# Kernel tuning notes

Hardware: AMD Instinct MI355X
Metric: run time of the kernel (lower is better)

The kernel has to match this reference:

```python
import jax, jax.numpy as jnp
import numpy as np

EPS = 1e-5

def setup_inputs() -> dict:
    key = jax.random.key(0)
    k1, k2 = jax.random.split(key)
    N, D = 8192, 256
    q_features = jax.random.normal(k1, (N, D), dtype=jnp.float32)
    g_features = jax.random.normal(k2, (N, D), dtype=jnp.float32)
    return {"q_features": q_features, "g_features": g_features}

def reference(q_features, g_features):
    # logits[i, j] = q_i . g_j ; original computes row i as g_features @ q_i
    logits = jnp.einsum('id,jd->ij', q_features, g_features)  # [N, N]
    # exp(l_ii)/sum_j exp(l_ij) == softmax row diagonal (stable form, same math)
    probs_diag = jnp.diagonal(jax.nn.softmax(logits, axis=-1))  # [N]
    loss = jnp.mean(-jnp.log(probs_diag + EPS))
    return loss
```

## Files before the change

kernel.cpp:

```cpp
#include <hip/hip_runtime.h>
#include <stdint.h>


#define LOG2E 1.44269504f
#define KOFF  92.3324826f

typedef __attribute__((ext_vector_type(8))) short short8;
typedef __attribute__((ext_vector_type(4))) float f32x4;

__device__ __forceinline__ uint32_t pack2bf(float lo, float hi) {
    return __builtin_amdgcn_perm(__float_as_uint(hi), __float_as_uint(lo), 0x07060302u);
}

__global__ __launch_bounds__(256) void k_cvt(const float* __restrict__ q,
                                             const float* __restrict__ g,
                                             uint4* __restrict__ qb,
                                             uint4* __restrict__ gb) {
    int o = blockIdx.x * 256 + threadIdx.x;
    const float* src = q;
    uint4* dst = qb;
    float s = LOG2E;
    if (o >= 262144) { o -= 262144; src = g; dst = gb; s = 1.0f; }
    int p   = o >> 11;
    int b   = (o >> 6) & 31;
    int l   = o & 63;
    int row = p * 64 + (b & 3) * 16 + (l & 15);
    int k0  = (b >> 2) * 32 + (l >> 4) * 8;
    const float4* sp = (const float4*)(src + row * 256 + k0);
    float4 a = sp[0], c = sp[1];
    uint4 ov;
    ov.x = pack2bf(a.x * s, a.y * s); ov.y = pack2bf(a.z * s, a.w * s);
    ov.z = pack2bf(c.x * s, c.y * s); ov.w = pack2bf(c.z * s, c.w * s);
    dst[o] = ov;
}

__global__ __launch_bounds__(256, 2) void k_main(const uint4* __restrict__ qb,
                                                 const uint4* __restrict__ gb,
                                                 float* __restrict__ zpart,
                                                 float* __restrict__ diag) {
    const int tid  = threadIdx.x;
    const int wave = tid >> 6;
    const int lane = tid & 63;
    const int l15  = lane & 15;
    const int quad = lane >> 4;
    const int t    = blockIdx.x >> 4;
    const int cs   = blockIdx.x & 15;
    const int rowbase = t * 256 + wave * 64;

    short8 afrag[4][8];
    {
        const char* qp = (const char*)qb + (size_t)(t * 4 + wave) * 32768 + (lane << 4);
#pragma unroll
        for (int rg = 0; rg < 4; ++rg)
#pragma unroll
            for (int ks = 0; ks < 8; ++ks)
                afrag[rg][ks] = *(const short8*)(qp + ((ks * 4 + rg) << 10));
    }

    float zacc[4][4];
#pragma unroll
    for (int rg = 0; rg < 4; ++rg)
#pragma unroll
        for (int r = 0; r < 4; ++r) zacc[rg][r] = 0.f;

    const bool bd = (cs == (t >> 1));

    for (int jt = 0; jt < 8; ++jt) {
        const char* gp = (const char*)gb + (size_t)(cs * 8 + jt) * 32768 + (lane << 4);

        f32x4 acc[4][4];
#pragma unroll
        for (int rg = 0; rg < 4; ++rg)
#pragma unroll
            for (int cf = 0; cf < 4; ++cf) acc[rg][cf] = (f32x4){0.f, 0.f, 0.f, 0.f};

#pragma unroll
        for (int ks = 0; ks < 8; ++ks)
#pragma unroll
            for (int cf = 0; cf < 4; ++cf) {
                short8 b = *(const short8*)(gp + ((ks * 4 + cf) << 10));
#pragma unroll
                for (int rg = 0; rg < 4; ++rg)
                    acc[rg][cf] = __builtin_amdgcn_mfma_f32_16x16x32_bf16(
                        afrag[rg][ks], b, acc[rg][cf], 0, 0, 0);
            }

#pragma unroll
        for (int rg = 0; rg < 4; ++rg)
#pragma unroll
            for (int r = 0; r < 4; ++r) {
                float e0 = __builtin_amdgcn_exp2f(acc[rg][0][r] - KOFF);
                float e1 = __builtin_amdgcn_exp2f(acc[rg][1][r] - KOFF);
                float e2 = __builtin_amdgcn_exp2f(acc[rg][2][r] - KOFF);
                float e3 = __builtin_amdgcn_exp2f(acc[rg][3][r] - KOFF);
                zacc[rg][r] += (e0 + e1) + (e2 + e3);
            }

        if (bd && ((jt >> 2) == (t & 1))) {
#pragma unroll
            for (int rg = 0; rg < 4; ++rg)
#pragma unroll
                for (int cf = 0; cf < 4; ++cf)
#pragma unroll
                    for (int r = 0; r < 4; ++r) {
                        int rowg = rowbase + rg * 16 + quad * 4 + r;
                        int colg = (cs << 9) + jt * 64 + cf * 16 + l15;
                        if (rowg == colg) diag[rowg] = acc[rg][cf][r];
                    }
        }
    }

#pragma unroll
    for (int d = 1; d < 16; d <<= 1)
#pragma unroll
        for (int rg = 0; rg < 4; ++rg)
#pragma unroll
            for (int r = 0; r < 4; ++r)
                zacc[rg][r] += __shfl_xor(zacc[rg][r], d, 64);

    if (l15 == 0) {
#pragma unroll
        for (int rg = 0; rg < 4; ++rg)
#pragma unroll
            for (int r = 0; r < 4; ++r)
                zpart[(rowbase + rg * 16 + quad * 4 + r) * 16 + cs] = zacc[rg][r];
    }
}

__global__ __launch_bounds__(256) void k_fin1(const float* __restrict__ zpart,
                                              const float* __restrict__ diag,
                                              float* __restrict__ partial) {
    __shared__ float red[4];
    int r = blockIdx.x * 256 + threadIdx.x;
    const float4* z = (const float4*)(zpart + r * 16);
    float4 a = z[0], b = z[1], c = z[2], d = z[3];
    float Z = (((a.x + a.y) + (a.z + a.w)) + ((b.x + b.y) + (b.z + b.w)))
            + (((c.x + c.y) + (c.z + c.w)) + ((d.x + d.y) + (d.z + d.w)));
    float p = __builtin_amdgcn_exp2f(diag[r] - KOFF) / Z;
    float v = -logf(p + 1e-5f);
#pragma unroll
    for (int dd = 1; dd < 64; dd <<= 1) v += __shfl_xor(v, dd, 64);
    if ((threadIdx.x & 63) == 0) red[threadIdx.x >> 6] = v;
    __syncthreads();
    if (threadIdx.x == 0)
        partial[blockIdx.x] = (red[0] + red[1]) + (red[2] + red[3]);
}

__global__ void k_fin2(const float* __restrict__ partial, float* __restrict__ out) {
    float v = (threadIdx.x < 32) ? partial[threadIdx.x] : 0.f;
#pragma unroll
    for (int d = 1; d < 32; d <<= 1) v += __shfl_xor(v, d, 64);
    if (threadIdx.x == 0) out[0] = v * (1.f / 8192.f);
}

extern "C" void kernel_launch(void* const* d_in, const int* in_sizes, int n_in,
                              void* d_out, int out_size, void* d_ws, size_t ws_size,
                              hipStream_t stream) {
    const float* q = (const float*)d_in[0];
    const float* g = (const float*)d_in[1];
    char* ws = (char*)d_ws;
    uint4* qb     = (uint4*)ws;
    uint4* gb     = (uint4*)(ws + (4u << 20));
    float* diag   = (float*)(ws + (8u << 20));
    float* zpart  = (float*)(ws + (8u << 20) + (32u << 10));
    float* partial= (float*)(ws + (8u << 20) + (576u << 10));
    k_cvt <<<2048, 256, 0, stream>>>(q, g, qb, gb);
    k_main<<<512,  256, 0, stream>>>(qb, gb, zpart, diag);
    k_fin1<<<32,   256, 0, stream>>>(zpart, diag, partial);
    k_fin2<<<1,     64, 0, stream>>>(partial, (float*)d_out);
    (void)in_sizes; (void)n_in; (void)out_size; (void)ws_size;
}
```

Measured before the change: 110.5 us.

## Halve row tile per block, stage half of G tiles through LDS, raise occupancy

Each block now covers 128 rows instead of 256, with waves pairing up so two waves share a 64-row Q panel across column halves, and the grid doubles to 1024 blocks with launch bounds allowing 4 blocks per CU. Half of each G tile is loaded into LDS via global_load_lds and shared across waves, while the other half is still read directly from global memory. Accumulators are initialized to -KOFF, which removes the per-element subtract before exp2, and the diagonal is stored with the offset already applied. The aim is lower register pressure, higher occupancy and less redundant G traffic. In exchange it adds two block barriers per tile and halves A-fragment reuse per B load.

```diff
diff --git a/kernel.cpp b/kernel.cpp
--- a/kernel.cpp
+++ b/kernel.cpp
@@ -7,6 +7,9 @@
 
 typedef __attribute__((ext_vector_type(8))) short short8;
 typedef __attribute__((ext_vector_type(4))) float f32x4;
+
+typedef __attribute__((address_space(1))) const uint32_t gu32;
+typedef __attribute__((address_space(3))) uint32_t lu32;
 
 __device__ __forceinline__ uint32_t pack2bf(float lo, float hi) {
     return __builtin_amdgcn_perm(__float_as_uint(hi), __float_as_uint(lo), 0x07060302u);
@@ -34,10 +37,11 @@
     dst[o] = ov;
 }
 
-__global__ __launch_bounds__(256, 2) void k_main(const uint4* __restrict__ qb,
+__global__ __launch_bounds__(256, 4) void k_main(const uint4* __restrict__ qb,
                                                  const uint4* __restrict__ gb,
                                                  float* __restrict__ zpart,
                                                  float* __restrict__ diag) {
+    __shared__ char lds[16384];
     const int tid  = threadIdx.x;
     const int wave = tid >> 6;
     const int lane = tid & 63;
@@ -45,82 +49,86 @@
     const int quad = lane >> 4;
     const int t    = blockIdx.x >> 4;
     const int cs   = blockIdx.x & 15;
-    const int rowbase = t * 256 + wave * 64;
+    const int rowbase = t * 128 + wave * 32;
 
-    short8 afrag[4][8];
+    short8 afrag[2][8];
     {
-        const char* qp = (const char*)qb + (size_t)(t * 4 + wave) * 32768 + (lane << 4);
+        const char* qp = (const char*)qb + (size_t)(t * 2 + (wave >> 1)) * 32768 + (lane << 4);
+        const int cfb = (wave & 1) * 2;
 #pragma unroll
-        for (int rg = 0; rg < 4; ++rg)
+        for (int rg = 0; rg < 2; ++rg)
 #pragma unroll
             for (int ks = 0; ks < 8; ++ks)
-                afrag[rg][ks] = *(const short8*)(qp + ((ks * 4 + rg) << 10));
+                afrag[rg][ks] = *(const short8*)(qp + ((ks * 4 + cfb + rg) << 10));
     }
 
-    float zacc[4][4];
+    float zacc[2][4];
 #pragma unroll
-    for (int rg = 0; rg < 4; ++rg)
+    for (int rg = 0; rg < 2; ++rg)
 #pragma unroll
         for (int r = 0; r < 4; ++r) zacc[rg][r] = 0.f;
 
-    const bool bd = (cs == (t >> 1));
+    const bool bd = (cs == (t >> 2));
 
     for (int jt = 0; jt < 8; ++jt) {
-        const char* gp = (const char*)gb + (size_t)(cs * 8 + jt) * 32768 + (lane << 4);
+        const char* gp  = (const char*)gb + (size_t)(cs * 8 + jt) * 32768;
+        const char* gpl = gp + (lane << 4);
+#pragma unroll
+        for (int i = 0; i < 4; ++i) {
+            int s  = wave * 4 + i;
+            int ks = s >> 1, cf = s & 1;
+            __builtin_amdgcn_global_load_lds(
+                (gu32*)(gp + ((ks * 4 + cf) << 10) + (lane << 4)),
+                (lu32*)(lds + (s << 10)), 16, 0, 0);
+        }
+        __syncthreads();
 
-        f32x4 acc[4][4];
+        const bool dj = bd && ((jt >> 1) == (t & 3));
 #pragma unroll
-        for (int rg = 0; rg < 4; ++rg)
+        for (int cf = 0; cf < 4; ++cf) {
+            f32x4 acc[2];
+            acc[0] = (f32x4){-KOFF, -KOFF, -KOFF, -KOFF};
+            acc[1] = acc[0];
 #pragma unroll
-            for (int cf = 0; cf < 4; ++cf) acc[rg][cf] = (f32x4){0.f, 0.f, 0.f, 0.f};
-
+            for (int ks = 0; ks < 8; ++ks) {
+                short8 b;
+                if (cf < 2)
+                    b = *(const short8*)(lds + ((ks * 2 + cf) << 10) + (lane << 4));
+                else
+                    b = *(const short8*)(gpl + ((ks * 4 + cf) << 10));
+                acc[0] = __builtin_amdgcn_mfma_f32_16x16x32_bf16(afrag[0][ks], b, acc[0], 0, 0, 0);
+                acc[1] = __builtin_amdgcn_mfma_f32_16x16x32_bf16(afrag[1][ks], b, acc[1], 0, 0, 0);
+            }
 #pragma unroll
-        for (int ks = 0; ks < 8; ++ks)
+            for (int rg = 0; rg < 2; ++rg)
 #pragma unroll
-            for (int cf = 0; cf < 4; ++cf) {
-                short8 b = *(const short8*)(gp + ((ks * 4 + cf) << 10));
+                for (int r = 0; r < 4; ++r)
+                    zacc[rg][r] += __builtin_amdgcn_exp2f(acc[rg][r]);
+            if (dj) {
 #pragma unroll
-                for (int rg = 0; rg < 4; ++rg)
-                    acc[rg][cf] = __builtin_amdgcn_mfma_f32_16x16x32_bf16(
-                        afrag[rg][ks], b, acc[rg][cf], 0, 0, 0);
-            }
-
-#pragma unroll
-        for (int rg = 0; rg < 4; ++rg)
-#pragma unroll
-            for (int r = 0; r < 4; ++r) {
-                float e0 = __builtin_amdgcn_exp2f(acc[rg][0][r] - KOFF);
-                float e1 = __builtin_amdgcn_exp2f(acc[rg][1][r] - KOFF);
-                float e2 = __builtin_amdgcn_exp2f(acc[rg][2][r] - KOFF);
-                float e3 = __builtin_amdgcn_exp2f(acc[rg][3][r] - KOFF);
-                zacc[rg][r] += (e0 + e1) + (e2 + e3);
-            }
-
-        if (bd && ((jt >> 2) == (t & 1))) {
-#pragma unroll
-            for (int rg = 0; rg < 4; ++rg)
-#pragma unroll
-                for (int cf = 0; cf < 4; ++cf)
+                for (int rg = 0; rg < 2; ++rg)
 #pragma unroll
                     for (int r = 0; r < 4; ++r) {
                         int rowg = rowbase + rg * 16 + quad * 4 + r;
                         int colg = (cs << 9) + jt * 64 + cf * 16 + l15;
-                        if (rowg == colg) diag[rowg] = acc[rg][cf][r];
+                        if (rowg == colg) diag[rowg] = acc[rg][r];
                     }
+            }
         }
+        __syncthreads();
     }
 
 #pragma unroll
     for (int d = 1; d < 16; d <<= 1)
 #pragma unroll
-        for (int rg = 0; rg < 4; ++rg)
+        for (int rg = 0; rg < 2; ++rg)
 #pragma unroll
             for (int r = 0; r < 4; ++r)
                 zacc[rg][r] += __shfl_xor(zacc[rg][r], d, 64);
 
     if (l15 == 0) {
 #pragma unroll
-        for (int rg = 0; rg < 4; ++rg)
+        for (int rg = 0; rg < 2; ++rg)
 #pragma unroll
             for (int r = 0; r < 4; ++r)
                 zpart[(rowbase + rg * 16 + quad * 4 + r) * 16 + cs] = zacc[rg][r];
@@ -136,7 +144,7 @@
     float4 a = z[0], b = z[1], c = z[2], d = z[3];
     float Z = (((a.x + a.y) + (a.z + a.w)) + ((b.x + b.y) + (b.z + b.w)))
             + (((c.x + c.y) + (c.z + c.w)) + ((d.x + d.y) + (d.z + d.w)));
-    float p = __builtin_amdgcn_exp2f(diag[r] - KOFF) / Z;
+    float p = __builtin_amdgcn_exp2f(diag[r]) / Z;
     float v = -logf(p + 1e-5f);
 #pragma unroll
     for (int dd = 1; dd < 64; dd <<= 1) v += __shfl_xor(v, dd, 64);
@@ -165,7 +173,7 @@
     float* zpart  = (float*)(ws + (8u << 20) + (32u << 10));
     float* partial= (float*)(ws + (8u << 20) + (576u << 10));
     k_cvt <<<2048, 256, 0, stream>>>(q, g, qb, gb);
-    k_main<<<512,  256, 0, stream>>>(qb, gb, zpart, diag);
+    k_main<<<1024, 256, 0, stream>>>(qb, gb, zpart, diag);
     k_fin1<<<32,   256, 0, stream>>>(zpart, diag, partial);
     k_fin2<<<1,     64, 0, stream>>>(partial, (float*)d_out);
     (void)in_sizes; (void)n_in; (void)out_size; (void)ws_size;
```

Result: slower. 289.7 us (+162.3%).

## Split block tile across 2x2 waves with double-buffered B fragments

Applied to the files above, without the earlier changes.

Each block now covers 128 rows instead of 256. Its four waves form a 2x2 grid (row half × column half), and the grid doubles to 1024 blocks. B fragments for 16-column slices are register double-buffered, so the next slice's loads overlap the current MFMAs. The KOFF offset is folded into the accumulator's initial value. The extra column split doubles the zpart partial sums, and the finisher now reduces 32 entries per row. In exchange, A-fragment reuse per B load drops, while occupancy and load/compute overlap increase.

```diff
diff --git a/kernel.cpp b/kernel.cpp
--- a/kernel.cpp
+++ b/kernel.cpp
@@ -40,16 +40,18 @@
                                                  float* __restrict__ diag) {
     const int tid  = threadIdx.x;
     const int wave = tid >> 6;
+    const int wr   = wave >> 1;
+    const int wc   = wave & 1;
     const int lane = tid & 63;
     const int l15  = lane & 15;
     const int quad = lane >> 4;
     const int t    = blockIdx.x >> 4;
     const int cs   = blockIdx.x & 15;
-    const int rowbase = t * 256 + wave * 64;
+    const int rowbase = t * 128 + wr * 64;
 
     short8 afrag[4][8];
     {
-        const char* qp = (const char*)qb + (size_t)(t * 4 + wave) * 32768 + (lane << 4);
+        const char* qp = (const char*)qb + (size_t)(t * 2 + wr) * 32768 + (lane << 4);
 #pragma unroll
         for (int rg = 0; rg < 4; ++rg)
 #pragma unroll
@@ -63,50 +65,49 @@
 #pragma unroll
         for (int r = 0; r < 4; ++r) zacc[rg][r] = 0.f;
 
-    const bool bd = (cs == (t >> 1));
+    const bool bd = (cs == (t >> 2));
+    const int  sd = (((t & 3) << 1) | wr) * 2;
 
-    for (int jt = 0; jt < 8; ++jt) {
-        const char* gp = (const char*)gb + (size_t)(cs * 8 + jt) * 32768 + (lane << 4);
+    const char* gpb = (const char*)gb + (size_t)(cs * 8) * 32768 + (wc << 11) + (lane << 4);
 
-        f32x4 acc[4][4];
+    short8 b0[8], b1[8];
 #pragma unroll
-        for (int rg = 0; rg < 4; ++rg)
+    for (int ks = 0; ks < 8; ++ks)
+        b0[ks] = *(const short8*)(gpb + (ks << 12));
+
 #pragma unroll
-            for (int cf = 0; cf < 4; ++cf) acc[rg][cf] = (f32x4){0.f, 0.f, 0.f, 0.f};
+    for (int s = 0; s < 16; ++s) {
+        const short8* cur = (s & 1) ? b1 : b0;
+        short8*       nxt = (s & 1) ? b0 : b1;
+        if (s < 15) {
+            const char* pn = gpb + (((s + 1) >> 1) * 32768) + (((s + 1) & 1) << 10);
+#pragma unroll
+            for (int ks = 0; ks < 8; ++ks)
+                nxt[ks] = *(const short8*)(pn + (ks << 12));
+        }
 
+        f32x4 acc[4];
+#pragma unroll
+        for (int rg = 0; rg < 4; ++rg) acc[rg] = (f32x4){-KOFF, -KOFF, -KOFF, -KOFF};
 #pragma unroll
         for (int ks = 0; ks < 8; ++ks)
 #pragma unroll
-            for (int cf = 0; cf < 4; ++cf) {
-                short8 b = *(const short8*)(gp + ((ks * 4 + cf) << 10));
-#pragma unroll
-                for (int rg = 0; rg < 4; ++rg)
-                    acc[rg][cf] = __builtin_amdgcn_mfma_f32_16x16x32_bf16(
-                        afrag[rg][ks], b, acc[rg][cf], 0, 0, 0);
-            }
+            for (int rg = 0; rg < 4; ++rg)
+                acc[rg] = __builtin_amdgcn_mfma_f32_16x16x32_bf16(
+                    afrag[rg][ks], cur[ks], acc[rg], 0, 0, 0);
 
 #pragma unroll
         for (int rg = 0; rg < 4; ++rg)
 #pragma unroll
-            for (int r = 0; r < 4; ++r) {
-                float e0 = __builtin_amdgcn_exp2f(acc[rg][0][r] - KOFF);
-                float e1 = __builtin_amdgcn_exp2f(acc[rg][1][r] - KOFF);
-                float e2 = __builtin_amdgcn_exp2f(acc[rg][2][r] - KOFF);
-                float e3 = __builtin_amdgcn_exp2f(acc[rg][3][r] - KOFF);
-                zacc[rg][r] += (e0 + e1) + (e2 + e3);
-            }
+            for (int r = 0; r < 4; ++r)
+                zacc[rg][r] += __builtin_amdgcn_exp2f(acc[rg][r]);
 
-        if (bd && ((jt >> 2) == (t & 1))) {
+        if (bd && (s >> 1) * 2 == sd) {
+            int rg = (wc << 1) | (s & 1);
 #pragma unroll
-            for (int rg = 0; rg < 4; ++rg)
-#pragma unroll
-                for (int cf = 0; cf < 4; ++cf)
-#pragma unroll
-                    for (int r = 0; r < 4; ++r) {
-                        int rowg = rowbase + rg * 16 + quad * 4 + r;
-                        int colg = (cs << 9) + jt * 64 + cf * 16 + l15;
-                        if (rowg == colg) diag[rowg] = acc[rg][cf][r];
-                    }
+            for (int r = 0; r < 4; ++r)
+                if (quad * 4 + r == l15)
+                    diag[rowbase + rg * 16 + l15] = acc[rg][r];
         }
     }
 
@@ -123,7 +124,7 @@
         for (int rg = 0; rg < 4; ++rg)
 #pragma unroll
             for (int r = 0; r < 4; ++r)
-                zpart[(rowbase + rg * 16 + quad * 4 + r) * 16 + cs] = zacc[rg][r];
+                zpart[(rowbase + rg * 16 + quad * 4 + r) * 32 + cs * 2 + wc] = zacc[rg][r];
     }
 }
 
@@ -132,11 +133,14 @@
                                               float* __restrict__ partial) {
     __shared__ float red[4];
     int r = blockIdx.x * 256 + threadIdx.x;
-    const float4* z = (const float4*)(zpart + r * 16);
-    float4 a = z[0], b = z[1], c = z[2], d = z[3];
-    float Z = (((a.x + a.y) + (a.z + a.w)) + ((b.x + b.y) + (b.z + b.w)))
-            + (((c.x + c.y) + (c.z + c.w)) + ((d.x + d.y) + (d.z + d.w)));
-    float p = __builtin_amdgcn_exp2f(diag[r] - KOFF) / Z;
+    const float4* z = (const float4*)(zpart + r * 32);
+    float Z = 0.f;
+#pragma unroll
+    for (int i = 0; i < 8; ++i) {
+        float4 a = z[i];
+        Z += (a.x + a.y) + (a.z + a.w);
+    }
+    float p = __builtin_amdgcn_exp2f(diag[r]) / Z;
     float v = -logf(p + 1e-5f);
 #pragma unroll
     for (int dd = 1; dd < 64; dd <<= 1) v += __shfl_xor(v, dd, 64);
@@ -163,9 +167,9 @@
     uint4* gb     = (uint4*)(ws + (4u << 20));
     float* diag   = (float*)(ws + (8u << 20));
     float* zpart  = (float*)(ws + (8u << 20) + (32u << 10));
-    float* partial= (float*)(ws + (8u << 20) + (576u << 10));
+    float* partial= (float*)(ws + (8u << 20) + (1056u << 10));
     k_cvt <<<2048, 256, 0, stream>>>(q, g, qb, gb);
-    k_main<<<512,  256, 0, stream>>>(qb, gb, zpart, diag);
+    k_main<<<1024, 256, 0, stream>>>(qb, gb, zpart, diag);
     k_fin1<<<32,   256, 0, stream>>>(zpart, diag, partial);
     k_fin2<<<1,     64, 0, stream>>>(partial, (float*)d_out);
     (void)in_sizes; (void)n_in; (void)out_size; (void)ws_size;
```

After: 151.7 us. 37.4% more time.
